# Optimization experiments

Measured on AMD Instinct MI355X. Metric: run time of the kernel, lower is better.

## Reference

```python
import jax, jax.numpy as jnp
import numpy as np

VOCAB = 1_000_000
EMB = 50
OUT = 2
BATCH = 128
SEQ = 2000


def setup_inputs() -> dict:
    key = jax.random.key(0)
    k1, k2, k3 = jax.random.split(key, 3)
    t = jax.random.randint(k1, (BATCH, SEQ), 0, VOCAB, dtype=jnp.int64)
    embeddings = jax.random.normal(k2, (VOCAB, EMB), dtype=jnp.float32) * 0.02
    # xavier_uniform for the linear layer, as in the torch init
    limit = float(np.sqrt(6.0 / (EMB + OUT)))
    W = jax.random.uniform(k3, (OUT, EMB), dtype=jnp.float32, minval=-limit, maxval=limit)
    b = jnp.zeros((OUT,), dtype=jnp.float32)
    return {"t": t, "embeddings": embeddings, "W": W, "b": b}


def reference(t, embeddings, W, b):
    # embedding-bag style sum pooling: skip -1 padding positions
    mask = (t != -1)                                   # [B, S]
    safe_idx = jnp.where(mask, t, 0)
    gathered = embeddings[safe_idx] * mask[..., None].astype(embeddings.dtype)  # [B, S, E]
    # original divides by len(t) == batch size (kept faithfully)
    pooled = gathered.sum(axis=1) / jnp.asarray(t.shape[0], embeddings.dtype)   # [B, E]
    res = pooled @ W.T + b                             # [B, OUT]
    return jax.nn.relu(res)
```

## Files before the change

kernel.cpp:

```cpp
#include <hip/hip_runtime.h>

#define BATCH 128
#define SEQ   2000
#define EMB   50
#define OUTD  2

#define CHUNKS 16
#define RPB    (SEQ / CHUNKS)
#define TPB    256
#define WAVES  (TPB / 64)

__global__ __launch_bounds__(TPB) void embbag_partial_kernel(
    const int* __restrict__ t,
    const float* __restrict__ emb,
    const float* __restrict__ W,
    float* __restrict__ partial)
{
    __shared__ float4 wl[EMB / 2];
    __shared__ float2 red[WAVES];

    const int tid = threadIdx.x;
    const int c = blockIdx.x;
    const int b = blockIdx.y;

    if (tid < EMB / 2) {
        wl[tid] = make_float4(W[2 * tid], W[2 * tid + 1],
                              W[EMB + 2 * tid], W[EMB + 2 * tid + 1]);
    }
    __syncthreads();

    float a0 = 0.0f, a1 = 0.0f;
    const int pair = tid >> 1;
    const int k    = tid & 1;
    if (pair < RPB) {
        const int s = c * RPB + pair;
        const int idx = t[b * SEQ + s];
        if (idx != -1) {
            const float2* __restrict__ row =
                (const float2*)(emb + (size_t)idx * EMB);
#pragma unroll
            for (int i = 0; i < 12; ++i) {
                float2 e = row[2 * i + k];
                float4 w = wl[2 * i + k];
                a0 = fmaf(e.x, w.x, fmaf(e.y, w.y, a0));
                a1 = fmaf(e.x, w.z, fmaf(e.y, w.w, a1));
            }
            if (k == 0) {
                float2 e = row[24];
                float4 w = wl[24];
                a0 = fmaf(e.x, w.x, fmaf(e.y, w.y, a0));
                a1 = fmaf(e.x, w.z, fmaf(e.y, w.w, a1));
            }
        }
    }

#pragma unroll
    for (int off = 32; off > 0; off >>= 1) {
        a0 += __shfl_down(a0, off, 64);
        a1 += __shfl_down(a1, off, 64);
    }
    const int wave = tid >> 6;
    const int lane = tid & 63;
    if (lane == 0) red[wave] = make_float2(a0, a1);
    __syncthreads();

    if (tid == 0) {
        float s0 = 0.0f, s1 = 0.0f;
#pragma unroll
        for (int w = 0; w < WAVES; ++w) { s0 += red[w].x; s1 += red[w].y; }
        float* p = partial + ((size_t)b * CHUNKS + c) * OUTD;
        p[0] = s0;
        p[1] = s1;
    }
}

__global__ __launch_bounds__(TPB) void finalize_kernel(
    const float* __restrict__ partial,
    const float* __restrict__ bias,
    float* __restrict__ out)
{
    const int i = threadIdx.x;
    if (i < BATCH * OUTD) {
        const int b = i >> 1;
        const int o = i & 1;
        float s = 0.0f;
#pragma unroll
        for (int c = 0; c < CHUNKS; ++c)
            s += partial[((size_t)b * CHUNKS + c) * OUTD + o];
        s = s * (1.0f / (float)BATCH) + bias[o];
        out[i] = fmaxf(s, 0.0f);
    }
}

extern "C" void kernel_launch(void* const* d_in, const int* in_sizes, int n_in,
                              void* d_out, int out_size, void* d_ws, size_t ws_size,
                              hipStream_t stream) {
    const int*   t    = (const int*)d_in[0];
    const float* emb  = (const float*)d_in[1];
    const float* W    = (const float*)d_in[2];
    const float* bias = (const float*)d_in[3];
    float* out        = (float*)d_out;
    float* partial    = (float*)d_ws;

    dim3 grid(CHUNKS, BATCH);
    embbag_partial_kernel<<<grid, TPB, 0, stream>>>(t, emb, W, partial);
    finalize_kernel<<<1, TPB, 0, stream>>>(partial, bias, out);
}
```

Baseline: 252.8 us.

## Gather each embedding row with a 32-lane group and stage indices in LDS

```diff
diff --git a/kernel.cpp b/kernel.cpp
--- a/kernel.cpp
+++ b/kernel.cpp
@@ -5,10 +5,14 @@
 #define EMB   50
 #define OUTD  2
 
-#define CHUNKS 16
+#define CHUNKS 25
 #define RPB    (SEQ / CHUNKS)
 #define TPB    256
 #define WAVES  (TPB / 64)
+#define GRP    32
+#define NGRP   (TPB / GRP)
+#define RPG    (RPB / NGRP)
+#define LPR    (EMB / 2)
 
 __global__ __launch_bounds__(TPB) void embbag_partial_kernel(
     const int* __restrict__ t,
@@ -16,41 +20,32 @@
     const float* __restrict__ W,
     float* __restrict__ partial)
 {
-    __shared__ float4 wl[EMB / 2];
+    __shared__ int sIdx[RPB];
     __shared__ float2 red[WAVES];
 
     const int tid = threadIdx.x;
     const int c = blockIdx.x;
     const int b = blockIdx.y;
 
-    if (tid < EMB / 2) {
-        wl[tid] = make_float4(W[2 * tid], W[2 * tid + 1],
-                              W[EMB + 2 * tid], W[EMB + 2 * tid + 1]);
-    }
+    if (tid < RPB) sIdx[tid] = t[b * SEQ + c * RPB + tid];
     __syncthreads();
 
+    const int g = tid >> 5;
+    const int j = tid & 31;
+
     float a0 = 0.0f, a1 = 0.0f;
-    const int pair = tid >> 1;
-    const int k    = tid & 1;
-    if (pair < RPB) {
-        const int s = c * RPB + pair;
-        const int idx = t[b * SEQ + s];
-        if (idx != -1) {
-            const float2* __restrict__ row =
-                (const float2*)(emb + (size_t)idx * EMB);
+    if (j < LPR) {
+        const float2 w0 = *(const float2*)(W + 2 * j);
+        const float2 w1 = *(const float2*)(W + EMB + 2 * j);
+        const int* gi = sIdx + g * RPG;
 #pragma unroll
-            for (int i = 0; i < 12; ++i) {
-                float2 e = row[2 * i + k];
-                float4 w = wl[2 * i + k];
-                a0 = fmaf(e.x, w.x, fmaf(e.y, w.y, a0));
-                a1 = fmaf(e.x, w.z, fmaf(e.y, w.w, a1));
-            }
-            if (k == 0) {
-                float2 e = row[24];
-                float4 w = wl[24];
-                a0 = fmaf(e.x, w.x, fmaf(e.y, w.y, a0));
-                a1 = fmaf(e.x, w.z, fmaf(e.y, w.w, a1));
-            }
+        for (int r = 0; r < RPG; ++r) {
+            const int idx = gi[r];
+            const size_t off = (size_t)((idx < 0) ? 0 : idx) * EMB + 2 * j;
+            float2 e = *(const float2*)(emb + off);
+            if (idx < 0) { e.x = 0.0f; e.y = 0.0f; }
+            a0 = fmaf(e.x, w0.x, fmaf(e.y, w0.y, a0));
+            a1 = fmaf(e.x, w1.x, fmaf(e.y, w1.y, a1));
         }
     }
 
@@ -85,8 +80,8 @@
         const int o = i & 1;
         float s = 0.0f;
 #pragma unroll
-        for (int c = 0; c < CHUNKS; ++c)
-            s += partial[((size_t)b * CHUNKS + c) * OUTD + o];
+        for (int cc = 0; cc < CHUNKS; ++cc)
+            s += partial[((size_t)b * CHUNKS + cc) * OUTD + o];
         s = s * (1.0f / (float)BATCH) + bias[o];
         out[i] = fmaxf(s, 0.0f);
     }
```

Result: no change. 253.1 us (+0.1%).
